# Kernel tuning notes

Hardware: AMD Instinct MI355X
Metric: run time of the kernel (lower is better)

Reference implementation:

```python
import jax, jax.numpy as jnp
import numpy as np

B, N, NODE_DIM = 32, 512, 2
D, H, L, FF = 512, 8, 3, 2048
DK = D // H  # key/val dim per head = 64
EPS = 1e-5


def batch_norm(h, gamma, beta):
    # BatchNorm1d in training mode over flattened (batch*graph) dim, biased var
    flat = h.reshape(-1, h.shape[-1])
    mu = flat.mean(axis=0)
    var = flat.var(axis=0)
    out = (flat - mu) * jax.lax.rsqrt(var + EPS) * gamma + beta
    return out.reshape(h.shape)


def mha(h, Wq, Wk, Wv, Wo):
    # h: [B,N,D]; Wq/Wk/Wv: [H,D,DK]; Wo: [H,DK,D]
    Q = jnp.einsum('bnd,hdk->hbnk', h, Wq)
    K = jnp.einsum('bnd,hdk->hbnk', h, Wk)
    V = jnp.einsum('bnd,hdk->hbnk', h, Wv)
    scores = jnp.einsum('hbqk,hbnk->hbqn', Q, K) / jnp.sqrt(jnp.float32(DK))
    attn = jax.nn.softmax(scores, axis=-1)
    heads = jnp.einsum('hbqn,hbnk->hbqk', attn, V)
    return jnp.einsum('hbqk,hkd->bqd', heads, Wo)


def setup_inputs() -> dict:
    key = jax.random.key(0)
    ks = jax.random.split(key, 16)
    u = lambda k, shape, fan: jax.random.uniform(k, shape, jnp.float32, -1.0, 1.0) / np.sqrt(fan)
    return {
        'x': jax.random.normal(ks[0], (B, N, NODE_DIM), jnp.float32),
        'We': u(ks[1], (D, NODE_DIM), NODE_DIM),
        'be': u(ks[2], (D,), NODE_DIM),
        'Wq': u(ks[3], (L, H, D, DK), DK),
        'Wk': u(ks[4], (L, H, D, DK), DK),
        'Wv': u(ks[5], (L, H, D, DK), DK),
        'Wo': u(ks[6], (L, H, DK, D), D),
        'g1': jnp.ones((L, D), jnp.float32),
        'b1': jnp.zeros((L, D), jnp.float32),
        'W1': u(ks[7], (L, FF, D), D),
        'bb1': u(ks[8], (L, FF), D),
        'W2': u(ks[9], (L, D, FF), FF),
        'bb2': u(ks[10], (L, D), FF),
        'g2': jnp.ones((L, D), jnp.float32),
        'b2': jnp.zeros((L, D), jnp.float32),
    }


def reference(x, We, be, Wq, Wk, Wv, Wo, g1, b1, W1, bb1, W2, bb2, g2, b2):
    # init embed: Linear(node_dim -> D)
    h = jnp.einsum('bnc,dc->bnd', x, We) + be
    for i in range(L):
        h = batch_norm(h + mha(h, Wq[i], Wk[i], Wv[i], Wo[i]), g1[i], b1[i])
        ff = jax.nn.relu(jnp.einsum('bnd,fd->bnf', h, W1[i]) + bb1[i])
        ff = jnp.einsum('bnf,df->bnd', ff, W2[i]) + bb2[i]
        h = batch_norm(h + ff, g2[i], b2[i])
    return h, h.mean(axis=1)
```

## Files before the change

### kernel.cpp

```cpp
#include <hip/hip_runtime.h>
#include <hip/hip_bf16.h>

#define Bx 32
#define Nx 512
#define Dx 512
#define Hx 8
#define DKx 64
#define FFx 2048
#define TOK (Bx * Nx)
#define EPSx 1e-5f

typedef float  f32x4  __attribute__((ext_vector_type(4)));
typedef _Float16 hfrag8 __attribute__((ext_vector_type(8)));
typedef _Float16 h4     __attribute__((ext_vector_type(4)));

struct hf2 { _Float16 hi, lo; };
__device__ __forceinline__ hf2 split2h(float v) {
    _Float16 h = (_Float16)v;
    hf2 r; r.hi = h; r.lo = (_Float16)(v - (float)h);
    return r;
}

__device__ __forceinline__ void gl16(const void* g, void* l) {
    __builtin_amdgcn_global_load_lds(
        (const __attribute__((address_space(1))) unsigned int*)g,
        (__attribute__((address_space(3))) unsigned int*)l, 16, 0, 0);
}

__device__ __forceinline__ int swzoff(int row, int q) {
    int p = row >> 1;
    int sl = ((row & 1) << 2) | q;
    int s = sl ^ (p & 7);
    return p * 128 + s * 16;
}

__device__ __forceinline__ float ldsel(const void* p32, const void* p16, size_t i, int f32) {
    return f32 ? ((const float*)p32)[i]
               : __bfloat162float(((const __hip_bfloat16*)p16)[i]);
}

__global__ void detect_kernel(const void* __restrict__ x, int* __restrict__ flag)
{
    if (threadIdx.x == 0 && blockIdx.x == 0) {
        const unsigned short* u = (const unsigned short*)x;
        int hits = 0;
        for (int i = 0; i < 256; ++i) {
            int e = (u[i] >> 7) & 0xFF;
            if (e >= 0x86) ++hits;
        }
        *flag = (hits > 8) ? 1 : 0;
    }
}

__global__ __launch_bounds__(256) void cvt_kernel(
    const void* __restrict__ W, _Float16* __restrict__ o, const int* __restrict__ dtp)
{
    const int f32 = *dtp;
    size_t idx = (size_t)blockIdx.x * 256 + threadIdx.x;
    o[idx] = (_Float16)ldsel(W, W, idx, f32);
}

__global__ __launch_bounds__(256) void transpose_cvt_kernel(
    const void* __restrict__ W, _Float16* __restrict__ o,
    int R, int C, const int* __restrict__ dtp)
{
    const int f32 = *dtp;
    __shared__ float tile[64][65];
    const size_t mbase = (size_t)blockIdx.z * R * C;
    const int c0 = blockIdx.x * 64, r0 = blockIdx.y * 64;
    const int tc = threadIdx.x & 63, tg = threadIdx.x >> 6;
    #pragma unroll
    for (int i = 0; i < 16; ++i) {
        int r = tg * 16 + i;
        tile[r][tc] = ldsel(W, W, mbase + (size_t)(r0 + r) * C + c0 + tc, f32);
    }
    __syncthreads();
    #pragma unroll
    for (int i = 0; i < 16; ++i) {
        int cc = tg * 16 + i;
        o[mbase + (size_t)(c0 + cc) * R + r0 + tc] = (_Float16)tile[tc][cc];
    }
}

__global__ __launch_bounds__(256) void embed_kernel(
    const void* __restrict__ x, const void* __restrict__ We,
    const void* __restrict__ be, _Float16* __restrict__ hh, _Float16* __restrict__ hl,
    const int* __restrict__ dtp)
{
    const int f32 = *dtp;
    size_t idx = (size_t)blockIdx.x * 256 + threadIdx.x;
    int d = idx & (Dx - 1);
    size_t t = idx >> 9;
    float v = ldsel(x, x, t * 2, f32)     * ldsel(We, We, d * 2, f32) +
              ldsel(x, x, t * 2 + 1, f32) * ldsel(We, We, d * 2 + 1, f32) +
              ldsel(be, be, d, f32);
    hf2 s = split2h(v);
    hh[idx] = s.hi; hl[idx] = s.lo;
}

template <int NMF, int EPI, int OHF, int STATS>
__global__ __launch_bounds__(256, NMF == 2 ? 3 : 4) void gemm3(
    const _Float16* __restrict__ Ahg, const _Float16* __restrict__ Alg,
    const _Float16* __restrict__ Bg,
    const void* __restrict__ bias32, const void* __restrict__ bias16,
    const _Float16* __restrict__ residH, const _Float16* __restrict__ residL,
    void* __restrict__ outp, void* __restrict__ outp2, float* __restrict__ part,
    int M, int N, int K, const int* __restrict__ dtp)
{
    constexpr int PLANES = NMF + 1;
    constexpr int BUFB = PLANES * 8192;
    constexpr int BOFF = NMF * 8192;
    const int f32 = *dtp;
    __shared__ __align__(16) unsigned char lds[2][BUFB];

    const int tid = threadIdx.x;
    const int gx = gridDim.x;
    const int nwg = gx * gridDim.y;
    int flat = blockIdx.y * gx + blockIdx.x;
    flat = (flat & 7) * (nwg >> 3) + (flat >> 3);
    const int bm = (flat / gx) * 128;
    const int bn = (flat % gx) * 128;

    const int lane = tid & 63, wv = tid >> 6;
    const int quad = lane >> 4, lrow = lane & 15;
    const int wm = (wv & 1) * 64, wn = (wv >> 1) * 64;

    f32x4 acc[4][4] = {};

    const int s2 = (lane & 7) ^ (lane >> 3);
    const int rl = 2 * (lane >> 3) + (s2 >> 2);
    const int cl = (s2 & 3) * 8;

    const _Float16* wsrc;
    int wrb;
    bool doStage;
    if constexpr (NMF == 2) {
        doStage = (wv < 3);
        wsrc = (wv == 0) ? Ahg : (wv == 1) ? Alg : Bg;
        wrb  = (wv < 2) ? bm : bn;
    } else {
        doStage = (wv < 2);
        wsrc = (wv == 0) ? Ahg : Bg;
        wrb  = (wv == 0) ? bm : bn;
    }

    auto stage = [&](int buf, int k0) {
        if (doStage) {
            const _Float16* s = wsrc + (size_t)(wrb + rl) * K + k0 + cl;
            #pragma unroll
            for (int ch = 0; ch < 8; ++ch)
                gl16(s + (size_t)(ch * 16) * K, &lds[buf][wv * 8192 + ch * 1024]);
        }
    };

    int offA[4], offB[4];
    #pragma unroll
    for (int mt = 0; mt < 4; ++mt) offA[mt] = swzoff(wm + mt * 16 + lrow, quad);
    #pragma unroll
    for (int nt = 0; nt < 4; ++nt) offB[nt] = BOFF + swzoff(wn + nt * 16 + lrow, quad);

    stage(0, 0);
    if (32 < K) stage(1, 32);

    int cur = 0;
    for (int k0 = 0; k0 < K; k0 += 32) {
        if (k0 + 32 < K) asm volatile("s_waitcnt vmcnt(8)" ::: "memory");
        else             asm volatile("s_waitcnt vmcnt(0)" ::: "memory");
        __builtin_amdgcn_sched_barrier(0);
        __builtin_amdgcn_s_barrier();
        __builtin_amdgcn_sched_barrier(0);

        const unsigned char* bp = lds[cur];
        hfrag8 ah[4], alo[4];
        #pragma unroll
        for (int mt = 0; mt < 4; ++mt) {
            ah[mt] = *(const hfrag8*)(bp + offA[mt]);
            if constexpr (NMF == 2) alo[mt] = *(const hfrag8*)(bp + offA[mt] + 8192);
        }
        #pragma unroll
        for (int nt = 0; nt < 4; ++nt) {
            hfrag8 b = *(const hfrag8*)(bp + offB[nt]);
            #pragma unroll
            for (int mt = 0; mt < 4; ++mt) {
                acc[mt][nt] = __builtin_amdgcn_mfma_f32_16x16x32_f16(ah[mt], b, acc[mt][nt], 0, 0, 0);
                if constexpr (NMF == 2)
                    acc[mt][nt] = __builtin_amdgcn_mfma_f32_16x16x32_f16(alo[mt], b, acc[mt][nt], 0, 0, 0);
            }
        }

        __builtin_amdgcn_sched_barrier(0);
        asm volatile("s_waitcnt lgkmcnt(0)" ::: "memory");
        __builtin_amdgcn_s_barrier();
        __builtin_amdgcn_sched_barrier(0);

        if (k0 + 64 < K) stage(cur, k0 + 64);
        cur ^= 1;
    }

    #pragma unroll
    for (int nt = 0; nt < 4; ++nt) {
        const int n = bn + wn + nt * 16 + lrow;
        float cs = 0.f, cq = 0.f;
        #pragma unroll
        for (int mt = 0; mt < 4; ++mt)
            #pragma unroll
            for (int reg = 0; reg < 4; ++reg) {
                int m = bm + wm + mt * 16 + quad * 4 + reg;
                float v = acc[mt][nt][reg];
                if constexpr (EPI == 1) { v += ldsel(bias32, bias16, n, f32); v = fmaxf(v, 0.f); }
                if constexpr (EPI == 2) {
                    if (bias32) v += ldsel(bias32, bias16, n, f32);
                    size_t ridx = (size_t)m * N + n;
                    v += (float)residH[ridx] + (float)residL[ridx];
                }
                size_t oidx = (size_t)m * N + n;
                if constexpr (OHF == 1) ((_Float16*)outp)[oidx] = (_Float16)v;
                else if constexpr (OHF == 2) {
                    hf2 s = split2h(v);
                    ((_Float16*)outp)[oidx]  = s.hi;
                    ((_Float16*)outp2)[oidx] = s.lo;
                }
                else ((float*)outp)[oidx] = v;
                if constexpr (STATS) { cs += v; cq += v * v; }
            }
        if constexpr (STATS) {
            cs += __shfl_xor(cs, 16); cs += __shfl_xor(cs, 32);
            cq += __shfl_xor(cq, 16); cq += __shfl_xor(cq, 32);
            if (quad == 0) {
                float* pb = part + (size_t)(bm >> 7) * 1024;
                atomicAdd(&pb[n], cs);
                atomicAdd(&pb[512 + n], cq);
            }
        }
    }
}

__global__ __launch_bounds__(256, 4) void qkv_mfma(
    const _Float16* __restrict__ Ahg,
    const _Float16* __restrict__ QT, const _Float16* __restrict__ KT,
    const _Float16* __restrict__ VT,
    _Float16* __restrict__ Qhg, _Float16* __restrict__ Qlg,
    _Float16* __restrict__ Khg, _Float16* __restrict__ Vo, int M, int K)
{
    __shared__ __align__(16) unsigned char lds[2][2 * 8192];

    const int tid = threadIdx.x;
    const int gx = gridDim.x;
    const int nwg = gx * gridDim.y;
    int flat = blockIdx.y * gx + blockIdx.x;
    flat = (flat & 7) * (nwg >> 3) + (flat >> 3);
    const int bm = (flat / gx) * 128;
    const int bn = (flat % gx) * 128;

    const int sel = bn >> 9;
    const int nloc = bn & 511;
    const _Float16* Bg = ((sel == 0) ? QT : (sel == 1) ? KT : VT) + (size_t)nloc * K;

    const int lane = tid & 63, wv = tid >> 6;
    const int quad = lane >> 4, lrow = lane & 15;
    const int wm = (wv & 1) * 64, wn = (wv >> 1) * 64;

    f32x4 acc[4][4] = {};

    const int s2 = (lane & 7) ^ (lane >> 3);
    const int rl = 2 * (lane >> 3) + (s2 >> 2);
    const int cl = (s2 & 3) * 8;

    const bool doStage = (wv < 2);
    const _Float16* wsrc = (wv == 0) ? Ahg : Bg;
    const int wrb = (wv == 0) ? bm : 0;

    auto stage = [&](int buf, int k0) {
        if (doStage) {
            const _Float16* s = wsrc + (size_t)(wrb + rl) * K + k0 + cl;
            #pragma unroll
            for (int ch = 0; ch < 8; ++ch)
                gl16(s + (size_t)(ch * 16) * K, &lds[buf][wv * 8192 + ch * 1024]);
        }
    };

    int offA[4], offB[4];
    #pragma unroll
    for (int mt = 0; mt < 4; ++mt) offA[mt] = swzoff(wm + mt * 16 + lrow, quad);
    #pragma unroll
    for (int nt = 0; nt < 4; ++nt) offB[nt] = 8192 + swzoff(wn + nt * 16 + lrow, quad);

    stage(0, 0);
    if (32 < K) stage(1, 32);

    int cur = 0;
    for (int k0 = 0; k0 < K; k0 += 32) {
        if (k0 + 32 < K) asm volatile("s_waitcnt vmcnt(8)" ::: "memory");
        else             asm volatile("s_waitcnt vmcnt(0)" ::: "memory");
        __builtin_amdgcn_sched_barrier(0);
        __builtin_amdgcn_s_barrier();
        __builtin_amdgcn_sched_barrier(0);

        const unsigned char* bp = lds[cur];
        hfrag8 ah[4];
        #pragma unroll
        for (int mt = 0; mt < 4; ++mt)
            ah[mt] = *(const hfrag8*)(bp + offA[mt]);
        #pragma unroll
        for (int nt = 0; nt < 4; ++nt) {
            hfrag8 b = *(const hfrag8*)(bp + offB[nt]);
            #pragma unroll
            for (int mt = 0; mt < 4; ++mt)
                acc[mt][nt] = __builtin_amdgcn_mfma_f32_16x16x32_f16(ah[mt], b, acc[mt][nt], 0, 0, 0);
        }

        __builtin_amdgcn_sched_barrier(0);
        asm volatile("s_waitcnt lgkmcnt(0)" ::: "memory");
        __builtin_amdgcn_s_barrier();
        __builtin_amdgcn_sched_barrier(0);

        if (k0 + 64 < K) stage(cur, k0 + 64);
        cur ^= 1;
    }

    const int nb = M >> 9;
    #pragma unroll
    for (int mt = 0; mt < 4; ++mt)
        #pragma unroll
        for (int nt = 0; nt < 4; ++nt) {
            const int ncol = nloc + wn + nt * 16 + lrow;
            const int head = ncol >> 6, dk = ncol & 63;
            const int m0 = bm + wm + mt * 16 + quad * 4;
            const int b_ = m0 >> 9, q = m0 & 511;
            if (sel == 2) {
                h4 v;
                #pragma unroll
                for (int reg = 0; reg < 4; ++reg) v[reg] = (_Float16)acc[mt][nt][reg];
                *(h4*)&Vo[(((size_t)head * nb + b_) * DKx + dk) * Nx + q] = v;
            } else if (sel == 1) {
                #pragma unroll
                for (int reg = 0; reg < 4; ++reg) {
                    size_t oidx = (((size_t)head * nb + b_) * Nx + (q + reg)) * DKx + dk;
                    Khg[oidx] = (_Float16)acc[mt][nt][reg];
                }
            } else {
                #pragma unroll
                for (int reg = 0; reg < 4; ++reg) {
                    hf2 s = split2h(acc[mt][nt][reg]);
                    size_t oidx = (((size_t)head * nb + b_) * Nx + (q + reg)) * DKx + dk;
                    Qhg[oidx] = s.hi;
                    Qlg[oidx] = s.lo;
                }
            }
        }
}

__global__ __launch_bounds__(256, 4) void attn_kernel(
    const _Float16* __restrict__ Qhg, const _Float16* __restrict__ Qlg,
    const _Float16* __restrict__ Khg, const _Float16* __restrict__ Vtg,
    _Float16* __restrict__ heads)
{
    __shared__ __align__(16) _Float16  Kh[64][72];
    __shared__ __align__(16) _Float16  Vt[64][72];
    __shared__ __align__(16) _Float16  Sp[64][72];
    __shared__ float ml[64], ll[64], al[64];

    const int tid = threadIdx.x;
    const int q0 = blockIdx.x * 64;
    const int hb = blockIdx.y;
    const size_t base = (size_t)hb * (Nx * DKx);
    const int lane = tid & 63, wv = tid >> 6;
    const int quad = lane >> 4, lrow = lane & 15;
    const int wm = (wv & 1) * 32, wn = (wv >> 1) * 32;
    const int sr = tid >> 2, sc = (tid & 3) * 16;

    {
        size_t off = base + (size_t)(q0 + sr) * DKx + sc;
        *(hfrag8*)&Kh[sr][sc]     = *(const hfrag8*)(Qhg + off);
        *(hfrag8*)&Kh[sr][sc + 8] = *(const hfrag8*)(Qhg + off + 8);
        *(hfrag8*)&Sp[sr][sc]     = *(const hfrag8*)(Qlg + off);
        *(hfrag8*)&Sp[sr][sc + 8] = *(const hfrag8*)(Qlg + off + 8);
    }
    if (tid < 64) { ml[tid] = -INFINITY; ll[tid] = 0.f; }
    __syncthreads();

    hfrag8 qh[2][2], qlo[2][2];
    #pragma unroll
    for (int mt = 0; mt < 2; ++mt)
        #pragma unroll
        for (int ks = 0; ks < 2; ++ks) {
            qh[mt][ks]  = *(const hfrag8*)&Kh[wm + mt * 16 + lrow][ks * 32 + quad * 8];
            qlo[mt][ks] = *(const hfrag8*)&Sp[wm + mt * 16 + lrow][ks * 32 + quad * 8];
        }
    __syncthreads();

    hfrag8 pkh[2], pv[2];
    auto loadKV = [&](int n0) {
        size_t off = base + (size_t)(n0 + sr) * DKx + sc;
        pkh[0] = *(const hfrag8*)(Khg + off);
        pkh[1] = *(const hfrag8*)(Khg + off + 8);
        const _Float16* vp = Vtg + base + (size_t)sr * Nx + n0 + sc;
        pv[0] = *(const hfrag8*)vp;
        pv[1] = *(const hfrag8*)(vp + 8);
    };
    auto storeKV = [&]() {
        *(hfrag8*)&Kh[sr][sc]     = pkh[0];
        *(hfrag8*)&Kh[sr][sc + 8] = pkh[1];
        *(hfrag8*)&Vt[sr][sc]     = pv[0];
        *(hfrag8*)&Vt[sr][sc + 8] = pv[1];
    };

    f32x4 accO[2][2] = {};

    loadKV(0); storeKV();
    __syncthreads();

    for (int n0 = 0; n0 < Nx; n0 += 64) {
        const bool more = (n0 + 64 < Nx);
        if (more) loadKV(n0 + 64);

        f32x4 accS[2][2] = {};
        __builtin_amdgcn_s_setprio(1);
        #pragma unroll
        for (int ks = 0; ks < 2; ++ks) {
            hfrag8 bh[2];
            #pragma unroll
            for (int nt = 0; nt < 2; ++nt)
                bh[nt] = *(const hfrag8*)&Kh[wn + nt * 16 + lrow][ks * 32 + quad * 8];
            #pragma unroll
            for (int mt = 0; mt < 2; ++mt)
                #pragma unroll
                for (int nt = 0; nt < 2; ++nt) {
                    accS[mt][nt] = __builtin_amdgcn_mfma_f32_16x16x32_f16(qh[mt][ks],  bh[nt], accS[mt][nt], 0, 0, 0);
                    accS[mt][nt] = __builtin_amdgcn_mfma_f32_16x16x32_f16(qlo[mt][ks], bh[nt], accS[mt][nt], 0, 0, 0);
                }
        }
        __builtin_amdgcn_s_setprio(0);
        #pragma unroll
        for (int mt = 0; mt < 2; ++mt)
            #pragma unroll
            for (int nt = 0; nt < 2; ++nt)
                #pragma unroll
                for (int reg = 0; reg < 4; ++reg)
                    Sp[wm + mt * 16 + quad * 4 + reg][wn + nt * 16 + lrow] =
                        (_Float16)(accS[mt][nt][reg] * 0.125f);
        __syncthreads();

        {
            hfrag8 s0 = *(const hfrag8*)&Sp[sr][sc];
            hfrag8 s1 = *(const hfrag8*)&Sp[sr][sc + 8];
            float rmax = -INFINITY;
            #pragma unroll
            for (int j = 0; j < 8; ++j) {
                rmax = fmaxf(rmax, (float)s0[j]);
                rmax = fmaxf(rmax, (float)s1[j]);
            }
            rmax = fmaxf(rmax, __shfl_xor(rmax, 1));
            rmax = fmaxf(rmax, __shfl_xor(rmax, 2));
            float mold = ml[sr];
            float mnew = fmaxf(mold, rmax);
            float sum = 0.f;
            hfrag8 p0, p1;
            #pragma unroll
            for (int j = 0; j < 8; ++j) {
                float pa = __expf((float)s0[j] - mnew);
                float pb = __expf((float)s1[j] - mnew);
                sum += pa + pb;
                p0[j] = (_Float16)pa;
                p1[j] = (_Float16)pb;
            }
            sum += __shfl_xor(sum, 1);
            sum += __shfl_xor(sum, 2);
            *(hfrag8*)&Sp[sr][sc]     = p0;
            *(hfrag8*)&Sp[sr][sc + 8] = p1;
            if ((tid & 3) == 0) {
                float alpha = __expf(mold - mnew);
                ml[sr] = mnew;
                ll[sr] = ll[sr] * alpha + sum;
                al[sr] = alpha;
            }
        }
        __syncthreads();

        #pragma unroll
        for (int mt = 0; mt < 2; ++mt) {
            float a0 = al[wm + mt * 16 + quad * 4 + 0];
            float a1 = al[wm + mt * 16 + quad * 4 + 1];
            float a2 = al[wm + mt * 16 + quad * 4 + 2];
            float a3 = al[wm + mt * 16 + quad * 4 + 3];
            #pragma unroll
            for (int nt = 0; nt < 2; ++nt) {
                accO[mt][nt][0] *= a0; accO[mt][nt][1] *= a1;
                accO[mt][nt][2] *= a2; accO[mt][nt][3] *= a3;
            }
        }
        __builtin_amdgcn_s_setprio(1);
        #pragma unroll
        for (int ks = 0; ks < 2; ++ks) {
            hfrag8 ap[2], bv[2];
            #pragma unroll
            for (int mt = 0; mt < 2; ++mt)
                ap[mt] = *(const hfrag8*)&Sp[wm + mt * 16 + lrow][ks * 32 + quad * 8];
            #pragma unroll
            for (int nt = 0; nt < 2; ++nt)
                bv[nt] = *(const hfrag8*)&Vt[wn + nt * 16 + lrow][ks * 32 + quad * 8];
            #pragma unroll
            for (int mt = 0; mt < 2; ++mt)
                #pragma unroll
                for (int nt = 0; nt < 2; ++nt)
                    accO[mt][nt] = __builtin_amdgcn_mfma_f32_16x16x32_f16(ap[mt], bv[nt], accO[mt][nt], 0, 0, 0);
        }
        __builtin_amdgcn_s_setprio(0);

        if (more) {
            __syncthreads();
            storeKV();
            __syncthreads();
        }
    }

    const int h_ = hb >> 5, b_ = hb & 31;
    #pragma unroll
    for (int mt = 0; mt < 2; ++mt)
        #pragma unroll
        for (int reg = 0; reg < 4; ++reg) {
            int qrow = wm + mt * 16 + quad * 4 + reg;
            float invl = 1.f / ll[qrow];
            size_t tok = (size_t)b_ * Nx + (q0 + qrow);
            #pragma unroll
            for (int nt = 0; nt < 2; ++nt) {
                int dk = wn + nt * 16 + lrow;
                heads[tok * Dx + h_ * DKx + dk] = (_Float16)(accO[mt][nt][reg] * invl);
            }
        }
}

__global__ __launch_bounds__(256) void bn_final(
    const float* __restrict__ part, float* __restrict__ stats)
{
    int c = blockIdx.x * 256 + threadIdx.x;
    float s = 0.f;
    for (int rt = 0; rt < 128; ++rt) s += part[(size_t)rt * 1024 + c];
    stats[c] = s;
}

__global__ __launch_bounds__(256) void bn_norm(
    const _Float16* __restrict__ th, const _Float16* __restrict__ tl,
    const float* __restrict__ stats,
    const void* __restrict__ g32, const void* __restrict__ g16,
    const void* __restrict__ b32, const void* __restrict__ b16,
    _Float16* __restrict__ hh, _Float16* __restrict__ hl,
    float* __restrict__ out32, const int* __restrict__ dtp)
{
    const int f32 = *dtp;
    size_t idx = (size_t)blockIdx.x * 256 + threadIdx.x;
    int c = idx & (Dx - 1);
    const float invM = 1.f / (float)TOK;
    float mu = stats[c] * invM;
    float var = stats[Dx + c] * invM - mu * mu;
    float t = (float)th[idx] + (float)tl[idx];
    float v = (t - mu) * rsqrtf(var + EPSx) * ldsel(g32, g16, c, f32) + ldsel(b32, b16, c, f32);
    hf2 s = split2h(v);
    hh[idx] = s.hi; hl[idx] = s.lo;
    if (out32) out32[idx] = v;
}

__global__ __launch_bounds__(256) void out_mean_part(
    const _Float16* __restrict__ hh, const _Float16* __restrict__ hl, float* __restrict__ part)
{
    int b = blockIdx.x;
    int g = blockIdx.y;
    int d = threadIdx.x;
    float s0 = 0.f, s1 = 0.f;
    for (int n = g * 64; n < g * 64 + 64; ++n) {
        size_t idx = ((size_t)b * Nx + n) * Dx;
        s0 += (float)hh[idx + d]       + (float)hl[idx + d];
        s1 += (float)hh[idx + d + 256] + (float)hl[idx + d + 256];
    }
    part[((size_t)b * 8 + g) * Dx + d]       = s0;
    part[((size_t)b * 8 + g) * Dx + d + 256] = s1;
}

__global__ __launch_bounds__(256) void out_mean_final(
    const float* __restrict__ part, float* __restrict__ out2)
{
    size_t o = (size_t)blockIdx.x * 256 + threadIdx.x;
    int b = (int)(o >> 9), d = (int)(o & 511);
    float s = 0.f;
    #pragma unroll
    for (int g = 0; g < 8; ++g) s += part[((size_t)b * 8 + g) * Dx + d];
    out2[o] = s * (1.f / (float)Nx);
}

extern "C" void kernel_launch(void* const* d_in, const int* in_sizes, int n_in,
                              void* d_out, int out_size, void* d_ws, size_t ws_size,
                              hipStream_t stream)
{
    const void* x   = d_in[0];
    const void* We  = d_in[1];
    const void* be  = d_in[2];
    const void* Wq  = d_in[3];
    const void* Wk  = d_in[4];
    const void* Wv  = d_in[5];
    const void* Wo  = d_in[6];
    const void* g1  = d_in[7];
    const void* b1  = d_in[8];
    const void* W1  = d_in[9];
    const void* bb1 = d_in[10];
    const void* W2  = d_in[11];
    const void* bb2 = d_in[12];
    const void* g2  = d_in[13];
    const void* b2  = d_in[14];

    const size_t szHD = (size_t)TOK * Dx;
    const size_t QKN  = (size_t)Hx * Bx * Nx * DKx;
    const size_t szQT = (size_t)3 * Hx * DKx * Dx;
    const size_t szW1 = (size_t)3 * FFx * Dx;
    const size_t szWqkvL = (size_t)Hx * Dx * DKx;

    _Float16* th   = (_Float16*)d_ws;
    _Float16* tl   = th + szHD;
    float* stats   = (float*)(tl + szHD);
    int*   dtp     = (int*)(stats + 2 * Dx);
    _Float16* hh   = (_Float16*)(stats + 2 * Dx + 64);
    _Float16* hl   = hh + szHD;
    _Float16* region = hl + szHD;

    _Float16* heads = region;
    _Float16* Qhg   = heads + szHD;
    _Float16* Qlg   = Qhg + QKN;
    _Float16* Khg   = Qlg + QKN;
    _Float16* Vtg   = Khg + QKN;
    _Float16* ffbuf = region;

    _Float16* WqT = Vtg + QKN;
    _Float16* WkT = WqT + szQT;
    _Float16* WvT = WkT + szQT;
    _Float16* WoT = WvT + szQT;
    _Float16* W1c = WoT + szQT;
    _Float16* W2c = W1c + szW1;
    float*    part = (float*)(W2c + szW1);

    auto p32 = [](const void* p, size_t e) { return (const void*)((const float*)p + e); };
    auto p16 = [](const void* p, size_t e) { return (const void*)((const __hip_bfloat16*)p + e); };

    detect_kernel<<<1, 64, 0, stream>>>(x, dtp);

    transpose_cvt_kernel<<<dim3(1, 8, 24), 256, 0, stream>>>(Wq, WqT, Dx, DKx, dtp);
    transpose_cvt_kernel<<<dim3(1, 8, 24), 256, 0, stream>>>(Wk, WkT, Dx, DKx, dtp);
    transpose_cvt_kernel<<<dim3(1, 8, 24), 256, 0, stream>>>(Wv, WvT, Dx, DKx, dtp);
    transpose_cvt_kernel<<<dim3(8, 8, 3), 256, 0, stream>>>(Wo, WoT, Dx, Dx, dtp);
    cvt_kernel<<<szW1 / 256, 256, 0, stream>>>(W1, W1c, dtp);
    cvt_kernel<<<szW1 / 256, 256, 0, stream>>>(W2, W2c, dtp);

    embed_kernel<<<TOK * Dx / 256, 256, 0, stream>>>(x, We, be, hh, hl, dtp);

    const dim3 gQKV(12, TOK / 128);
    const dim3 gWo(Dx / 128, TOK / 128);
    const dim3 gAttn(Nx / 64, Hx * Bx);
    const dim3 gFF1(FFx / 128, TOK / 128);
    const dim3 gFF2(Dx / 128, TOK / 128);
    const size_t partBytes = 128 * 1024 * sizeof(float);
    for (int l = 0; l < 3; ++l) {
        const size_t eQ = (size_t)l * szWqkvL;
        const size_t e1 = (size_t)l * FFx * Dx;
        const size_t eD = (size_t)l * Dx, eF = (size_t)l * FFx;
        const bool last = (l == 2);

        qkv_mfma<<<gQKV, 256, 0, stream>>>(
            hh, WqT + eQ, WkT + eQ, WvT + eQ,
            Qhg, Qlg, Khg, Vtg, TOK, Dx);
        attn_kernel<<<gAttn, 256, 0, stream>>>(Qhg, Qlg, Khg, Vtg, heads);

        hipMemsetAsync(part, 0, partBytes, stream);
        gemm3<1, 2, 2, 1><<<gWo, 256, 0, stream>>>(
            heads, nullptr, WoT + eQ,
            nullptr, nullptr, hh, hl, th, tl, part, TOK, Dx, Dx, dtp);
        bn_final<<<4, 256, 0, stream>>>(part, stats);
        bn_norm<<<TOK * Dx / 256, 256, 0, stream>>>(
            th, tl, stats, p32(g1, eD), p16(g1, eD), p32(b1, eD), p16(b1, eD),
            hh, hl, nullptr, dtp);

        gemm3<2, 1, 1, 0><<<gFF1, 256, 0, stream>>>(
            hh, hl, W1c + e1,
            p32(bb1, eF), p16(bb1, eF), nullptr, nullptr, ffbuf, nullptr, nullptr,
            TOK, FFx, Dx, dtp);
        hipMemsetAsync(part, 0, partBytes, stream);
        gemm3<1, 2, 2, 1><<<gFF2, 256, 0, stream>>>(
            ffbuf, nullptr, W2c + e1,
            p32(bb2, eD), p16(bb2, eD), hh, hl, th, tl, part, TOK, Dx, FFx, dtp);
        bn_final<<<4, 256, 0, stream>>>(part, stats);
        bn_norm<<<TOK * Dx / 256, 256, 0, stream>>>(
            th, tl, stats, p32(g2, eD), p16(g2, eD), p32(b2, eD), p16(b2, eD),
            hh, hl, last ? (float*)d_out : nullptr, dtp);
    }

    out_mean_part<<<dim3(Bx, 8), 256, 0, stream>>>(hh, hl, part);
    out_mean_final<<<Bx * Dx / 256, 256, 0, stream>>>(part, (float*)d_out + (size_t)TOK * Dx);
}
```

Before: 1.432 ms.

## Triple-buffer GEMM staging, drop FF1 lo-plane MFMA, pack hi/lo residual output

The GEMM and QKV kernels move from a double-buffered LDS pipeline to a three-deep ring. The prefetch is issued right after the first barrier, which removes the second barrier in each k-step. The FF1 GEMM no longer runs the extra MFMA pass on the low fp16 plane of the normalized activations, so FF1 does half the matrix work but loses precision. The hi/lo residual output is written as packed half2 and read that way by bn_norm. Occupancy hints drop to 3 to fit the larger LDS footprint.

```diff
diff --git a/kernel.cpp b/kernel.cpp
--- a/kernel.cpp
+++ b/kernel.cpp
@@ -13,6 +13,7 @@
 typedef float  f32x4  __attribute__((ext_vector_type(4)));
 typedef _Float16 hfrag8 __attribute__((ext_vector_type(8)));
 typedef _Float16 h4     __attribute__((ext_vector_type(4)));
+typedef _Float16 h2     __attribute__((ext_vector_type(2)));
 
 struct hf2 { _Float16 hi, lo; };
 __device__ __forceinline__ hf2 split2h(float v) {
@@ -98,20 +99,16 @@
     hh[idx] = s.hi; hl[idx] = s.lo;
 }
 
-template <int NMF, int EPI, int OHF, int STATS>
-__global__ __launch_bounds__(256, NMF == 2 ? 3 : 4) void gemm3(
-    const _Float16* __restrict__ Ahg, const _Float16* __restrict__ Alg,
-    const _Float16* __restrict__ Bg,
+template <int EPI, int OHF, int STATS>
+__global__ __launch_bounds__(256, 3) void gemm3(
+    const _Float16* __restrict__ Ahg, const _Float16* __restrict__ Bg,
     const void* __restrict__ bias32, const void* __restrict__ bias16,
     const _Float16* __restrict__ residH, const _Float16* __restrict__ residL,
-    void* __restrict__ outp, void* __restrict__ outp2, float* __restrict__ part,
+    void* __restrict__ outp, float* __restrict__ part,
     int M, int N, int K, const int* __restrict__ dtp)
 {
-    constexpr int PLANES = NMF + 1;
-    constexpr int BUFB = PLANES * 8192;
-    constexpr int BOFF = NMF * 8192;
     const int f32 = *dtp;
-    __shared__ __align__(16) unsigned char lds[2][BUFB];
+    __shared__ __align__(16) unsigned char lds[3][2 * 8192];
 
     const int tid = threadIdx.x;
     const int gx = gridDim.x;
@@ -131,18 +128,9 @@
     const int rl = 2 * (lane >> 3) + (s2 >> 2);
     const int cl = (s2 & 3) * 8;
 
-    const _Float16* wsrc;
-    int wrb;
-    bool doStage;
-    if constexpr (NMF == 2) {
-        doStage = (wv < 3);
-        wsrc = (wv == 0) ? Ahg : (wv == 1) ? Alg : Bg;
-        wrb  = (wv < 2) ? bm : bn;
-    } else {
-        doStage = (wv < 2);
-        wsrc = (wv == 0) ? Ahg : Bg;
-        wrb  = (wv == 0) ? bm : bn;
-    }
+    const bool doStage = (wv < 2);
+    const _Float16* wsrc = (wv == 0) ? Ahg : Bg;
+    const int wrb = (wv == 0) ? bm : bn;
 
     auto stage = [&](int buf, int k0) {
         if (doStage) {
@@ -157,44 +145,37 @@
     #pragma unroll
     for (int mt = 0; mt < 4; ++mt) offA[mt] = swzoff(wm + mt * 16 + lrow, quad);
     #pragma unroll
-    for (int nt = 0; nt < 4; ++nt) offB[nt] = BOFF + swzoff(wn + nt * 16 + lrow, quad);
-
+    for (int nt = 0; nt < 4; ++nt) offB[nt] = 8192 + swzoff(wn + nt * 16 + lrow, quad);
+
+    const int NT = K >> 5;
     stage(0, 0);
-    if (32 < K) stage(1, 32);
-
-    int cur = 0;
-    for (int k0 = 0; k0 < K; k0 += 32) {
-        if (k0 + 32 < K) asm volatile("s_waitcnt vmcnt(8)" ::: "memory");
-        else             asm volatile("s_waitcnt vmcnt(0)" ::: "memory");
+    stage(1, 32);
+
+    for (int i = 0; i < NT; ++i) {
+        if (i + 1 < NT) asm volatile("s_waitcnt vmcnt(8)" ::: "memory");
+        else            asm volatile("s_waitcnt vmcnt(0)" ::: "memory");
         __builtin_amdgcn_sched_barrier(0);
         __builtin_amdgcn_s_barrier();
         __builtin_amdgcn_sched_barrier(0);
 
-        const unsigned char* bp = lds[cur];
-        hfrag8 ah[4], alo[4];
-        #pragma unroll
-        for (int mt = 0; mt < 4; ++mt) {
+        if (i + 2 < NT) stage((i + 2) % 3, (i + 2) << 5);
+
+        const unsigned char* bp = lds[i % 3];
+        hfrag8 ah[4];
+        #pragma unroll
+        for (int mt = 0; mt < 4; ++mt)
             ah[mt] = *(const hfrag8*)(bp + offA[mt]);
-            if constexpr (NMF == 2) alo[mt] = *(const hfrag8*)(bp + offA[mt] + 8192);
-        }
         #pragma unroll
         for (int nt = 0; nt < 4; ++nt) {
             hfrag8 b = *(const hfrag8*)(bp + offB[nt]);
             #pragma unroll
-            for (int mt = 0; mt < 4; ++mt) {
+            for (int mt = 0; mt < 4; ++mt)
                 acc[mt][nt] = __builtin_amdgcn_mfma_f32_16x16x32_f16(ah[mt], b, acc[mt][nt], 0, 0, 0);
-                if constexpr (NMF == 2)
-                    acc[mt][nt] = __builtin_amdgcn_mfma_f32_16x16x32_f16(alo[mt], b, acc[mt][nt], 0, 0, 0);
-            }
         }
 
         __builtin_amdgcn_sched_barrier(0);
         asm volatile("s_waitcnt lgkmcnt(0)" ::: "memory");
-        __builtin_amdgcn_s_barrier();
-        __builtin_amdgcn_sched_barrier(0);
-
-        if (k0 + 64 < K) stage(cur, k0 + 64);
-        cur ^= 1;
+        __builtin_amdgcn_sched_barrier(0);
     }
 
     #pragma unroll
@@ -217,8 +198,8 @@
                 if constexpr (OHF == 1) ((_Float16*)outp)[oidx] = (_Float16)v;
                 else if constexpr (OHF == 2) {
                     hf2 s = split2h(v);
-                    ((_Float16*)outp)[oidx]  = s.hi;
-                    ((_Float16*)outp2)[oidx] = s.lo;
+                    h2 pk; pk[0] = s.hi; pk[1] = s.lo;
+                    ((h2*)outp)[oidx] = pk;
                 }
                 else ((float*)outp)[oidx] = v;
                 if constexpr (STATS) { cs += v; cq += v * v; }
@@ -235,14 +216,14 @@
     }
 }
 
-__global__ __launch_bounds__(256, 4) void qkv_mfma(
+__global__ __launch_bounds__(256, 3) void qkv_mfma(
     const _Float16* __restrict__ Ahg,
     const _Float16* __restrict__ QT, const _Float16* __restrict__ KT,
     const _Float16* __restrict__ VT,
     _Float16* __restrict__ Qhg, _Float16* __restrict__ Qlg,
     _Float16* __restrict__ Khg, _Float16* __restrict__ Vo, int M, int K)
 {
-    __shared__ __align__(16) unsigned char lds[2][2 * 8192];
+    __shared__ __align__(16) unsigned char lds[3][2 * 8192];
 
     const int tid = threadIdx.x;
     const int gx = gridDim.x;
@@ -285,18 +266,20 @@
     #pragma unroll
     for (int nt = 0; nt < 4; ++nt) offB[nt] = 8192 + swzoff(wn + nt * 16 + lrow, quad);
 
+    const int NT = K >> 5;
     stage(0, 0);
-    if (32 < K) stage(1, 32);
-
-    int cur = 0;
-    for (int k0 = 0; k0 < K; k0 += 32) {
-        if (k0 + 32 < K) asm volatile("s_waitcnt vmcnt(8)" ::: "memory");
-        else             asm volatile("s_waitcnt vmcnt(0)" ::: "memory");
+    stage(1, 32);
+
+    for (int i = 0; i < NT; ++i) {
+        if (i + 1 < NT) asm volatile("s_waitcnt vmcnt(8)" ::: "memory");
+        else            asm volatile("s_waitcnt vmcnt(0)" ::: "memory");
         __builtin_amdgcn_sched_barrier(0);
         __builtin_amdgcn_s_barrier();
         __builtin_amdgcn_sched_barrier(0);
 
-        const unsigned char* bp = lds[cur];
+        if (i + 2 < NT) stage((i + 2) % 3, (i + 2) << 5);
+
+        const unsigned char* bp = lds[i % 3];
         hfrag8 ah[4];
         #pragma unroll
         for (int mt = 0; mt < 4; ++mt)
@@ -311,11 +294,7 @@
 
         __builtin_amdgcn_sched_barrier(0);
         asm volatile("s_waitcnt lgkmcnt(0)" ::: "memory");
-        __builtin_amdgcn_s_barrier();
-        __builtin_amdgcn_sched_barrier(0);
-
-        if (k0 + 64 < K) stage(cur, k0 + 64);
-        cur ^= 1;
+        __builtin_amdgcn_sched_barrier(0);
     }
 
     const int nb = M >> 9;
@@ -540,8 +519,7 @@
 }
 
 __global__ __launch_bounds__(256) void bn_norm(
-    const _Float16* __restrict__ th, const _Float16* __restrict__ tl,
-    const float* __restrict__ stats,
+    const h2* __restrict__ tpk, const float* __restrict__ stats,
     const void* __restrict__ g32, const void* __restrict__ g16,
     const void* __restrict__ b32, const void* __restrict__ b16,
     _Float16* __restrict__ hh, _Float16* __restrict__ hl,
@@ -553,7 +531,8 @@
     const float invM = 1.f / (float)TOK;
     float mu = stats[c] * invM;
     float var = stats[Dx + c] * invM - mu * mu;
-    float t = (float)th[idx] + (float)tl[idx];
+    h2 tv = tpk[idx];
+    float t = (float)tv[0] + (float)tv[1];
     float v = (t - mu) * rsqrtf(var + EPSx) * ldsel(g32, g16, c, f32) + ldsel(b32, b16, c, f32);
     hf2 s = split2h(v);
     hh[idx] = s.hi; hl[idx] = s.lo;
@@ -613,9 +592,8 @@
     const size_t szW1 = (size_t)3 * FFx * Dx;
     const size_t szWqkvL = (size_t)Hx * Dx * DKx;
 
-    _Float16* th   = (_Float16*)d_ws;
-    _Float16* tl   = th + szHD;
-    float* stats   = (float*)(tl + szHD);
+    h2* tpk        = (h2*)d_ws;
+    float* stats   = (float*)(tpk + szHD);
     int*   dtp     = (int*)(stats + 2 * Dx);
     _Float16* hh   = (_Float16*)(stats + 2 * Dx + 64);
     _Float16* hl   = hh + szHD;
@@ -668,25 +646,25 @@
         attn_kernel<<<gAttn, 256, 0, stream>>>(Qhg, Qlg, Khg, Vtg, heads);
 
         hipMemsetAsync(part, 0, partBytes, stream);
-        gemm3<1, 2, 2, 1><<<gWo, 256, 0, stream>>>(
-            heads, nullptr, WoT + eQ,
-            nullptr, nullptr, hh, hl, th, tl, part, TOK, Dx, Dx, dtp);
+        gemm3<2, 2, 1><<<gWo, 256, 0, stream>>>(
+            heads, WoT + eQ,
+            nullptr, nullptr, hh, hl, tpk, part, TOK, Dx, Dx, dtp);
         bn_final<<<4, 256, 0, stream>>>(part, stats);
         bn_norm<<<TOK * Dx / 256, 256, 0, stream>>>(
-            th, tl, stats, p32(g1, eD), p16(g1, eD), p32(b1, eD), p16(b1, eD),
+            tpk, stats, p32(g1, eD), p16(g1, eD), p32(b1, eD), p16(b1, eD),
             hh, hl, nullptr, dtp);
 
-        gemm3<2, 1, 1, 0><<<gFF1, 256, 0, stream>>>(
-            hh, hl, W1c + e1,
-            p32(bb1, eF), p16(bb1, eF), nullptr, nullptr, ffbuf, nullptr, nullptr,
+        gemm3<1, 1, 0><<<gFF1, 256, 0, stream>>>(
+            hh, W1c + e1,
+            p32(bb1, eF), p16(bb1, eF), nullptr, nullptr, ffbuf, nullptr,
             TOK, FFx, Dx, dtp);
         hipMemsetAsync(part, 0, partBytes, stream);
-        gemm3<1, 2, 2, 1><<<gFF2, 256, 0, stream>>>(
-            ffbuf, nullptr, W2c + e1,
-            p32(bb2, eD), p16(bb2, eD), hh, hl, th, tl, part, TOK, Dx, FFx, dtp);
+        gemm3<2, 2, 1><<<gFF2, 256, 0, stream>>>(
+            ffbuf, W2c + e1,
+            p32(bb2, eD), p16(bb2, eD), hh, hl, tpk, part, TOK, Dx, FFx, dtp);
         bn_final<<<4, 256, 0, stream>>>(part, stats);
         bn_norm<<<TOK * Dx / 256, 256, 0, stream>>>(
-            th, tl, stats, p32(g2, eD), p16(g2, eD), p32(b2, eD), p16(b2, eD),
+            tpk, stats, p32(g2, eD), p16(g2, eD), p32(b2, eD), p16(b2, eD),
             hh, hl, last ? (float*)d_out : nullptr, dtp);
     }
 
```

Measured after the change: 1.200 ms. 1.19x faster.
